# Kernel optimization log

Measured on AMD Instinct MI355X. Metric: run time of the kernel, lower is better.

Reference implementation:

```python
import jax, jax.numpy as jnp
import numpy as np

B, T, OBS, H, A, S = 4096, 64, 64, 64, 8, 201


def setup_inputs() -> dict:
    key = jax.random.key(0)
    ks = jax.random.split(key, 13)
    n = lambda k, shp, s=1.0: jax.random.normal(k, shp, dtype=jnp.float32) * s
    return {
        "x": n(ks[0], (B, T, OBS)),
        "stack": jnp.zeros((B, S, H), jnp.float32),
        "stack_ptrs": jax.random.randint(ks[1], (B, 1), 0, 100, dtype=jnp.int32),
        # core_network: init.normal_(std=1.0) per source
        "W1": n(ks[2], (H, OBS + H)), "b1": n(ks[3], (H,)),
        "W2": n(ks[4], (H, H)), "b2": n(ks[5], (H,)),
        # stack_head: default torch Linear init ~ U(-1/sqrt(H), 1/sqrt(H))
        "Ws": (jax.random.uniform(ks[6], (3, H), dtype=jnp.float32) * 2 - 1) / np.sqrt(H),
        "bs": (jax.random.uniform(ks[7], (3,), dtype=jnp.float32) * 2 - 1) / np.sqrt(H),
        # policy/value heads: init.normal_(std=0.01)
        "Wp": n(ks[8], (A, H), 0.01), "bp": n(ks[9], (A,), 0.01),
        "Wv": n(ks[10], (1, H), 0.01), "bv": n(ks[11], (1,), 0.01),
    }


def reference(x, stack, stack_ptrs, W1, b1, W2, b2, Ws, bs, Wp, bp, Wv, bv):
    # x: [B,T,OBS]  stack: [B,S,H]  stack_ptrs: [B,1] int
    batch = x.shape[0]
    bidx = jnp.arange(batch)
    ptrs0 = stack_ptrs.astype(jnp.int32)[:, 0]  # [B]

    def step(carry, x_t):
        stk, ptrs = carry
        top = stk[bidx, ptrs]                                   # [B,H] gather at ptr
        h = jnp.tanh(jnp.concatenate([x_t, top], axis=1) @ W1.T + b1)
        p = jnp.tanh(h @ W2.T + b2)                             # [B,H]
        probs = jax.nn.softmax(p @ Ws.T + bs, axis=1)           # [B,3]
        ops = jnp.argmax(probs, axis=1).astype(jnp.int32)       # 0=pop,1=noop,2=push
        push = (ops == 2)[:, None]
        # conditional scatter: write p at row ptr only where op==2
        stk = stk.at[bidx, ptrs].set(jnp.where(push, p, top))
        ptrs = jnp.maximum(ptrs + ops - 1, 0)
        logits = p @ Wp.T + bp                                  # [B,A]
        value = (p @ Wv.T + bv)[:, 0]                           # [B]
        return (stk, ptrs), (logits, value)

    (stack_out, ptrs_out), (logits_t, values_t) = jax.lax.scan(
        step, (stack, ptrs0), jnp.swapaxes(x, 0, 1))
    logitss = jnp.swapaxes(logits_t, 0, 1)      # [B,T,A]
    values = values_t.reshape(-1)               # time-major [T*B], matching torch layout
    return logitss, values, stack_out, ptrs_out[:, None]
```

## Files before the change

### kernel.cpp

```cpp
#include <hip/hip_runtime.h>
#include <cstddef>

#define NB 4096
#define NT 64
#define NOBS 64
#define NH 64
#define NA 8
#define NS 201


__device__ __forceinline__ float bl(float v, int k) {
    return __int_as_float(__builtin_amdgcn_readlane(__float_as_int(v), k));
}

__launch_bounds__(64, 2)
__global__ void stacknet_kernel(const float* __restrict__ x,
                                const float* __restrict__ stack_in,
                                const int* __restrict__ ptrs_in,
                                const float* __restrict__ W1,
                                const float* __restrict__ b1,
                                const float* __restrict__ W2,
                                const float* __restrict__ b2,
                                const float* __restrict__ Ws,
                                const float* __restrict__ bs,
                                const float* __restrict__ Wp,
                                const float* __restrict__ bp,
                                const float* __restrict__ Wv,
                                const float* __restrict__ bv,
                                float* __restrict__ logits_out,
                                float* __restrict__ values_out,
                                float* __restrict__ stack,
                                float* __restrict__ ptrs_out) {
    const int lane = threadIdx.x;
    const int jb0  = blockIdx.x * 2;
    const int jb1  = jb0 + 1;
    const int aa   = lane & 15;

    __shared__ float xcl0[28 * NH];
    __shared__ float xcl1[28 * NH];
    __shared__ __align__(16) float shw[16 * 68];
    __shared__ __align__(16) float vb0[64];
    __shared__ __align__(16) float vb1[64];

    const float* xb0 = x + (size_t)jb0 * NT * NOBS;
    const float* xb1 = x + (size_t)jb1 * NT * NOBS;
    float* stk0 = stack + (size_t)jb0 * NS * NH;
    float* stk1 = stack + (size_t)jb1 * NS * NH;

    for (int i = lane; i < 16 * 64; i += 64) {
        int a = i >> 6, k = i & 63;
        float w = (a < 3) ? Ws[a * 64 + k]
                : (a < 11) ? Wp[(a - 3) * 64 + k]
                : (a == 11) ? Wv[k] : 0.f;
        shw[a * 68 + k] = w;
    }

    {
        const float4* s40 = (const float4*)(stack_in + (size_t)jb0 * NS * NH);
        const float4* s41 = (const float4*)(stack_in + (size_t)jb1 * NS * NH);
        float4* d40 = (float4*)stk0;
        float4* d41 = (float4*)stk1;
#pragma unroll 4
        for (int i = lane; i < 164 * 16; i += 64) { d40[i] = s40[i]; d41[i] = s41[i]; }
        if (lane < 16) {
            d40[3200 + lane] = s40[3200 + lane];
            d41[3200 + lane] = s41[3200 + lane];
        }
    }

    {
        float w1x[64];
#pragma unroll
        for (int j = 0; j < 16; ++j) {
            float4 w = ((const float4*)W1)[lane * 32 + j];
            w1x[4*j] = w.x; w1x[4*j+1] = w.y; w1x[4*j+2] = w.z; w1x[4*j+3] = w.w;
        }
        float xv0 = xb0[lane], xv1 = xb1[lane];
#pragma unroll 1
        for (int t = 0; t < NT; ++t) {
            float xn0 = (t + 1 < NT) ? xb0[(t + 1) * 64 + lane] : 0.f;
            float xn1 = (t + 1 < NT) ? xb1[(t + 1) * 64 + lane] : 0.f;
            vb0[lane] = xv0;
            vb1[lane] = xv1;
            float a0 = 0.f, a1 = 0.f;
            const float4* v40 = (const float4*)vb0;
            const float4* v41 = (const float4*)vb1;
#pragma unroll
            for (int j = 0; j < 16; ++j) {
                float4 q0 = v40[j], q1 = v41[j];
                a0 = fmaf(w1x[4*j],   q0.x, a0); a1 = fmaf(w1x[4*j],   q1.x, a1);
                a0 = fmaf(w1x[4*j+1], q0.y, a0); a1 = fmaf(w1x[4*j+1], q1.y, a1);
                a0 = fmaf(w1x[4*j+2], q0.z, a0); a1 = fmaf(w1x[4*j+2], q1.z, a1);
                a0 = fmaf(w1x[4*j+3], q0.w, a0); a1 = fmaf(w1x[4*j+3], q1.w, a1);
            }
            if (t < 28) {
                xcl0[t * 64 + lane] = a0;
                xcl1[t * 64 + lane] = a1;
            } else {
                stk0[(136 + t) * 64 + lane] = a0;
                stk1[(136 + t) * 64 + lane] = a1;
            }
            xv0 = xn0; xv1 = xn1;
        }
    }

    float w1h[64], w2r[64];
#pragma unroll
    for (int j = 0; j < 16; ++j) {
        float4 wa = ((const float4*)W1)[lane * 32 + 16 + j];
        w1h[4*j] = wa.x; w1h[4*j+1] = wa.y; w1h[4*j+2] = wa.z; w1h[4*j+3] = wa.w;
        float4 wb = ((const float4*)W2)[lane * 16 + j];
        w2r[4*j] = wb.x; w2r[4*j+1] = wb.y; w2r[4*j+2] = wb.z; w2r[4*j+3] = wb.w;
    }
    float b1r  = b1[lane];
    float b2r  = b2[lane];
    float shba = (aa < 3) ? bs[aa] : (aa < 11) ? bp[aa - 3] : (aa == 11) ? bv[0] : 0.f;

    asm volatile("s_waitcnt vmcnt(0)" ::: "memory");

    int ptr0 = ptrs_in[jb0], ptr1 = ptrs_in[jb1];
    float top0 = stk0[ptr0 * 64 + lane];
    float top1 = stk1[ptr1 * 64 + lane];
    int   lA0 = -1, lA0b = -1, lA0c = -1, lA1 = -1, lA1b = -1, lA1c = -1;
    float lV0 = 0.f, lV0b = 0.f, lV0c = 0.f, lV1 = 0.f, lV1b = 0.f, lV1c = 0.f;

    float* lgb0 = logits_out + (size_t)jb0 * NT * NA;
    float* lgb1 = logits_out + (size_t)jb1 * NT * NA;

    int r00 = (ptr0 > 0) ? (ptr0 - 1) : 0;
    int r01 = (ptr1 > 0) ? (ptr1 - 1) : 0;
    float c00 = stk0[r00 * 64 + lane], c20 = stk0[(ptr0 + 1) * 64 + lane];
    float c01 = stk1[r01 * 64 + lane], c21 = stk1[(ptr1 + 1) * 64 + lane];
    float xcv0 = xcl0[lane], xcv1 = xcl1[lane];

    const float4* shwa4 = (const float4*)(shw + aa * 68);

#pragma unroll 1
    for (int t = 0; t < NT; ++t) {
        vb0[lane] = top0;
        vb1[lane] = top1;
        float acc0 = xcv0, acc1 = xcv1;
        {
            const float4* v40 = (const float4*)vb0;
            const float4* v41 = (const float4*)vb1;
#pragma unroll
            for (int j = 0; j < 16; ++j) {
                float4 q0 = v40[j], q1 = v41[j];
                acc0 = fmaf(w1h[4*j],   q0.x, acc0); acc1 = fmaf(w1h[4*j],   q1.x, acc1);
                acc0 = fmaf(w1h[4*j+1], q0.y, acc0); acc1 = fmaf(w1h[4*j+1], q1.y, acc1);
                acc0 = fmaf(w1h[4*j+2], q0.z, acc0); acc1 = fmaf(w1h[4*j+2], q1.z, acc1);
                acc0 = fmaf(w1h[4*j+3], q0.w, acc0); acc1 = fmaf(w1h[4*j+3], q1.w, acc1);
            }
        }
        float h0 = tanhf(acc0 + b1r), h1 = tanhf(acc1 + b1r);

        vb0[lane] = h0;
        vb1[lane] = h1;
        float ac20 = 0.f, ac21 = 0.f;
        {
            const float4* v40 = (const float4*)vb0;
            const float4* v41 = (const float4*)vb1;
#pragma unroll
            for (int j = 0; j < 16; ++j) {
                float4 q0 = v40[j], q1 = v41[j];
                ac20 = fmaf(w2r[4*j],   q0.x, ac20); ac21 = fmaf(w2r[4*j],   q1.x, ac21);
                ac20 = fmaf(w2r[4*j+1], q0.y, ac20); ac21 = fmaf(w2r[4*j+1], q1.y, ac21);
                ac20 = fmaf(w2r[4*j+2], q0.z, ac20); ac21 = fmaf(w2r[4*j+2], q1.z, ac21);
                ac20 = fmaf(w2r[4*j+3], q0.w, ac20); ac21 = fmaf(w2r[4*j+3], q1.w, ac21);
            }
        }
        float p0 = tanhf(ac20 + b2r), p1 = tanhf(ac21 + b2r);

        vb0[lane] = p0;
        vb1[lane] = p1;
        float hc0 = 0.f, hc1 = 0.f;
        {
            const float4* v40 = (const float4*)vb0;
            const float4* v41 = (const float4*)vb1;
#pragma unroll
            for (int j = 0; j < 16; ++j) {
                float4 wq = shwa4[j];
                float4 q0 = v40[j], q1 = v41[j];
                hc0 = fmaf(q0.x, wq.x, hc0); hc1 = fmaf(q1.x, wq.x, hc1);
                hc0 = fmaf(q0.y, wq.y, hc0); hc1 = fmaf(q1.y, wq.y, hc1);
                hc0 = fmaf(q0.z, wq.z, hc0); hc1 = fmaf(q1.z, wq.z, hc1);
                hc0 = fmaf(q0.w, wq.w, hc0); hc1 = fmaf(q1.w, wq.w, hc1);
            }
        }
        float sv0 = hc0 + shba, sv1 = hc1 + shba;

        int op0, op1;
        {
            float s0 = bl(sv0, 0), s1 = bl(sv0, 1), s2 = bl(sv0, 2);
            float mx = fmaxf(fmaxf(s0, s1), s2);
            float e0 = expf(s0 - mx), e1 = expf(s1 - mx), e2 = expf(s2 - mx);
            float S = (e0 + e1) + e2;
            float q0 = e0 / S, q1 = e1 / S, q2 = e2 / S;
            op0 = 0; float pm = q0;
            if (q1 > pm) { pm = q1; op0 = 1; }
            if (q2 > pm) { op0 = 2; }
        }
        {
            float s0 = bl(sv1, 0), s1 = bl(sv1, 1), s2 = bl(sv1, 2);
            float mx = fmaxf(fmaxf(s0, s1), s2);
            float e0 = expf(s0 - mx), e1 = expf(s1 - mx), e2 = expf(s2 - mx);
            float S = (e0 + e1) + e2;
            float q0 = e0 / S, q1 = e1 / S, q2 = e2 / S;
            op1 = 0; float pm = q0;
            if (q1 > pm) { pm = q1; op1 = 1; }
            if (q2 > pm) { op1 = 2; }
        }

        int np0 = ptr0 + op0 - 1; np0 = (np0 < 0) ? 0 : np0;
        int np1 = ptr1 + op1 - 1; np1 = (np1 < 0) ? 0 : np1;

        int nr00 = (np0 > 0) ? (np0 - 1) : 0;
        int nr01 = (np1 > 0) ? (np1 - 1) : 0;
        float nc00 = stk0[nr00 * 64 + lane];
        float nc20 = stk0[(np0 + 1) * 64 + lane];
        float nc01 = stk1[nr01 * 64 + lane];
        float nc21 = stk1[(np1 + 1) * 64 + lane];
        int tn = t + 1;
        float nxcv0, nxcv1;
        if (tn < 28) {
            nxcv0 = xcl0[tn * 64 + lane];
            nxcv1 = xcl1[tn * 64 + lane];
        } else {
            nxcv0 = stk0[(136 + tn) * 64 + lane];
            nxcv1 = stk1[(136 + tn) * 64 + lane];
        }

        if (op0 == 2) stk0[ptr0 * 64 + lane] = p0;
        if (op1 == 2) stk1[ptr1 * 64 + lane] = p1;

        float sel0;
        if (op0 == 0)
            sel0 = (r00 == lA0) ? lV0 : (r00 == lA0b) ? lV0b
                 : (r00 == lA0c) ? lV0c : c00;
        else if (op0 == 1) sel0 = top0;
        else {
            int r2 = ptr0 + 1;
            sel0 = (r2 == lA0) ? lV0 : (r2 == lA0b) ? lV0b
                 : (r2 == lA0c) ? lV0c : c20;
        }
        if (op0 == 2) { lA0c = lA0b; lV0c = lV0b; lA0b = lA0; lV0b = lV0;
                        lA0 = ptr0; lV0 = p0; }

        float sel1;
        if (op1 == 0)
            sel1 = (r01 == lA1) ? lV1 : (r01 == lA1b) ? lV1b
                 : (r01 == lA1c) ? lV1c : c01;
        else if (op1 == 1) sel1 = top1;
        else {
            int r2 = ptr1 + 1;
            sel1 = (r2 == lA1) ? lV1 : (r2 == lA1b) ? lV1b
                 : (r2 == lA1c) ? lV1c : c21;
        }
        if (op1 == 2) { lA1c = lA1b; lV1c = lV1b; lA1b = lA1; lV1b = lV1;
                        lA1 = ptr1; lV1 = p1; }

        ptr0 = np0; top0 = sel0; r00 = nr00; c00 = nc00; c20 = nc20; xcv0 = nxcv0;
        ptr1 = np1; top1 = sel1; r01 = nr01; c01 = nc01; c21 = nc21; xcv1 = nxcv1;

        if (lane >= 3 && lane <= 10) {
            lgb0[t * NA + (lane - 3)] = sv0;
            lgb1[t * NA + (lane - 3)] = sv1;
        }
        if (lane == 11) {
            values_out[(size_t)t * NB + jb0] = sv0;
            values_out[(size_t)t * NB + jb1] = sv1;
        }
    }
    if (lane == 0) {
        ptrs_out[jb0] = (float)ptr0;
        ptrs_out[jb1] = (float)ptr1;
    }

    {
        const float4* s40 = (const float4*)(stack_in + (size_t)jb0 * NS * NH);
        const float4* s41 = (const float4*)(stack_in + (size_t)jb1 * NS * NH);
        float4* d40 = (float4*)stk0;
        float4* d41 = (float4*)stk1;
#pragma unroll
        for (int i = lane; i < 576; i += 64) {
            d40[2624 + i] = s40[2624 + i];
            d41[2624 + i] = s41[2624 + i];
        }
    }
}

extern "C" void kernel_launch(void* const* d_in, const int* in_sizes, int n_in,
                              void* d_out, int out_size, void* d_ws, size_t ws_size,
                              hipStream_t stream) {
    const float* x        = (const float*)d_in[0];
    const float* stack_in = (const float*)d_in[1];
    const int*   ptrs_in  = (const int*)d_in[2];
    const float* W1 = (const float*)d_in[3];
    const float* b1 = (const float*)d_in[4];
    const float* W2 = (const float*)d_in[5];
    const float* b2 = (const float*)d_in[6];
    const float* Ws = (const float*)d_in[7];
    const float* bs = (const float*)d_in[8];
    const float* Wp = (const float*)d_in[9];
    const float* bp = (const float*)d_in[10];
    const float* Wv = (const float*)d_in[11];
    const float* bv = (const float*)d_in[12];

    float* out      = (float*)d_out;
    float* logits   = out;
    float* values   = out + 2097152;
    float* stack    = out + 2359296;
    float* ptrs_out = out + 55050240;

    stacknet_kernel<<<NB / 2, 64, 0, stream>>>(x, stack_in, ptrs_in,
                                               W1, b1, W2, b2, Ws, bs,
                                               Wp, bp, Wv, bv,
                                               logits, values, stack, ptrs_out);
}
```

Baseline: 701.1 us.

## Skew the two batch rows' recurrences so their serial stages interleave

The main loop now runs row 0 and row 1 out of phase: each fused matvec pass pairs one row's layer stage with a different stage of the other row (W2 with W1, head with W2, W1 with head). The per-step dependency chain of one row can then overlap with independent work from the other instead of both rows waiting on the same tanh/softmax/readlane points. The x-projection prologue also reads x directly from global memory with float4 loads instead of staging it through LDS, unrolled by two. The risks are higher register pressure, a longer loop body, and direct global loads in the prologue.

```diff
diff --git a/kernel.cpp b/kernel.cpp
--- a/kernel.cpp
+++ b/kernel.cpp
@@ -75,19 +75,14 @@
             float4 w = ((const float4*)W1)[lane * 32 + j];
             w1x[4*j] = w.x; w1x[4*j+1] = w.y; w1x[4*j+2] = w.z; w1x[4*j+3] = w.w;
         }
-        float xv0 = xb0[lane], xv1 = xb1[lane];
-#pragma unroll 1
+#pragma unroll 2
         for (int t = 0; t < NT; ++t) {
-            float xn0 = (t + 1 < NT) ? xb0[(t + 1) * 64 + lane] : 0.f;
-            float xn1 = (t + 1 < NT) ? xb1[(t + 1) * 64 + lane] : 0.f;
-            vb0[lane] = xv0;
-            vb1[lane] = xv1;
+            const float4* xr0 = (const float4*)(xb0 + t * 64);
+            const float4* xr1 = (const float4*)(xb1 + t * 64);
             float a0 = 0.f, a1 = 0.f;
-            const float4* v40 = (const float4*)vb0;
-            const float4* v41 = (const float4*)vb1;
 #pragma unroll
             for (int j = 0; j < 16; ++j) {
-                float4 q0 = v40[j], q1 = v41[j];
+                float4 q0 = xr0[j], q1 = xr1[j];
                 a0 = fmaf(w1x[4*j],   q0.x, a0); a1 = fmaf(w1x[4*j],   q1.x, a1);
                 a0 = fmaf(w1x[4*j+1], q0.y, a0); a1 = fmaf(w1x[4*j+1], q1.y, a1);
                 a0 = fmaf(w1x[4*j+2], q0.z, a0); a1 = fmaf(w1x[4*j+2], q1.z, a1);
@@ -100,7 +95,6 @@
                 stk0[(136 + t) * 64 + lane] = a0;
                 stk1[(136 + t) * 64 + lane] = a1;
             }
-            xv0 = xn0; xv1 = xn1;
         }
     }
 
@@ -135,45 +129,45 @@
 
     const float4* shwa4 = (const float4*)(shw + aa * 68);
 
+    float h0;
+    {
+        vb0[lane] = top0;
+        float acc0 = xcv0;
+        const float4* v40 = (const float4*)vb0;
+#pragma unroll
+        for (int j = 0; j < 16; ++j) {
+            float4 q0 = v40[j];
+            acc0 = fmaf(w1h[4*j],   q0.x, acc0);
+            acc0 = fmaf(w1h[4*j+1], q0.y, acc0);
+            acc0 = fmaf(w1h[4*j+2], q0.z, acc0);
+            acc0 = fmaf(w1h[4*j+3], q0.w, acc0);
+        }
+        h0 = tanhf(acc0 + b1r);
+    }
+
 #pragma unroll 1
     for (int t = 0; t < NT; ++t) {
-        vb0[lane] = top0;
+        vb0[lane] = h0;
         vb1[lane] = top1;
-        float acc0 = xcv0, acc1 = xcv1;
+        float ac20 = 0.f, acc1 = xcv1;
         {
             const float4* v40 = (const float4*)vb0;
             const float4* v41 = (const float4*)vb1;
 #pragma unroll
             for (int j = 0; j < 16; ++j) {
                 float4 q0 = v40[j], q1 = v41[j];
-                acc0 = fmaf(w1h[4*j],   q0.x, acc0); acc1 = fmaf(w1h[4*j],   q1.x, acc1);
-                acc0 = fmaf(w1h[4*j+1], q0.y, acc0); acc1 = fmaf(w1h[4*j+1], q1.y, acc1);
-                acc0 = fmaf(w1h[4*j+2], q0.z, acc0); acc1 = fmaf(w1h[4*j+2], q1.z, acc1);
-                acc0 = fmaf(w1h[4*j+3], q0.w, acc0); acc1 = fmaf(w1h[4*j+3], q1.w, acc1);
-            }
-        }
-        float h0 = tanhf(acc0 + b1r), h1 = tanhf(acc1 + b1r);
-
-        vb0[lane] = h0;
+                ac20 = fmaf(w2r[4*j],   q0.x, ac20); acc1 = fmaf(w1h[4*j],   q1.x, acc1);
+                ac20 = fmaf(w2r[4*j+1], q0.y, ac20); acc1 = fmaf(w1h[4*j+1], q1.y, acc1);
+                ac20 = fmaf(w2r[4*j+2], q0.z, ac20); acc1 = fmaf(w1h[4*j+2], q1.z, acc1);
+                ac20 = fmaf(w2r[4*j+3], q0.w, ac20); acc1 = fmaf(w1h[4*j+3], q1.w, acc1);
+            }
+        }
+        float p0 = tanhf(ac20 + b2r);
+        float h1 = tanhf(acc1 + b1r);
+
+        vb0[lane] = p0;
         vb1[lane] = h1;
-        float ac20 = 0.f, ac21 = 0.f;
-        {
-            const float4* v40 = (const float4*)vb0;
-            const float4* v41 = (const float4*)vb1;
-#pragma unroll
-            for (int j = 0; j < 16; ++j) {
-                float4 q0 = v40[j], q1 = v41[j];
-                ac20 = fmaf(w2r[4*j],   q0.x, ac20); ac21 = fmaf(w2r[4*j],   q1.x, ac21);
-                ac20 = fmaf(w2r[4*j+1], q0.y, ac20); ac21 = fmaf(w2r[4*j+1], q1.y, ac21);
-                ac20 = fmaf(w2r[4*j+2], q0.z, ac20); ac21 = fmaf(w2r[4*j+2], q1.z, ac21);
-                ac20 = fmaf(w2r[4*j+3], q0.w, ac20); ac21 = fmaf(w2r[4*j+3], q1.w, ac21);
-            }
-        }
-        float p0 = tanhf(ac20 + b2r), p1 = tanhf(ac21 + b2r);
-
-        vb0[lane] = p0;
-        vb1[lane] = p1;
-        float hc0 = 0.f, hc1 = 0.f;
+        float hc0 = 0.f, ac21 = 0.f;
         {
             const float4* v40 = (const float4*)vb0;
             const float4* v41 = (const float4*)vb1;
@@ -181,15 +175,16 @@
             for (int j = 0; j < 16; ++j) {
                 float4 wq = shwa4[j];
                 float4 q0 = v40[j], q1 = v41[j];
-                hc0 = fmaf(q0.x, wq.x, hc0); hc1 = fmaf(q1.x, wq.x, hc1);
-                hc0 = fmaf(q0.y, wq.y, hc0); hc1 = fmaf(q1.y, wq.y, hc1);
-                hc0 = fmaf(q0.z, wq.z, hc0); hc1 = fmaf(q1.z, wq.z, hc1);
-                hc0 = fmaf(q0.w, wq.w, hc0); hc1 = fmaf(q1.w, wq.w, hc1);
-            }
-        }
-        float sv0 = hc0 + shba, sv1 = hc1 + shba;
-
-        int op0, op1;
+                hc0 = fmaf(q0.x, wq.x, hc0); ac21 = fmaf(w2r[4*j],   q1.x, ac21);
+                hc0 = fmaf(q0.y, wq.y, hc0); ac21 = fmaf(w2r[4*j+1], q1.y, ac21);
+                hc0 = fmaf(q0.z, wq.z, hc0); ac21 = fmaf(w2r[4*j+2], q1.z, ac21);
+                hc0 = fmaf(q0.w, wq.w, hc0); ac21 = fmaf(w2r[4*j+3], q1.w, ac21);
+            }
+        }
+        float sv0 = hc0 + shba;
+        float p1 = tanhf(ac21 + b2r);
+
+        int op0;
         {
             float s0 = bl(sv0, 0), s1 = bl(sv0, 1), s2 = bl(sv0, 2);
             float mx = fmaxf(fmaxf(s0, s1), s2);
@@ -200,38 +195,16 @@
             if (q1 > pm) { pm = q1; op0 = 1; }
             if (q2 > pm) { op0 = 2; }
         }
-        {
-            float s0 = bl(sv1, 0), s1 = bl(sv1, 1), s2 = bl(sv1, 2);
-            float mx = fmaxf(fmaxf(s0, s1), s2);
-            float e0 = expf(s0 - mx), e1 = expf(s1 - mx), e2 = expf(s2 - mx);
-            float S = (e0 + e1) + e2;
-            float q0 = e0 / S, q1 = e1 / S, q2 = e2 / S;
-            op1 = 0; float pm = q0;
-            if (q1 > pm) { pm = q1; op1 = 1; }
-            if (q2 > pm) { op1 = 2; }
-        }
-
         int np0 = ptr0 + op0 - 1; np0 = (np0 < 0) ? 0 : np0;
-        int np1 = ptr1 + op1 - 1; np1 = (np1 < 0) ? 0 : np1;
 
         int nr00 = (np0 > 0) ? (np0 - 1) : 0;
-        int nr01 = (np1 > 0) ? (np1 - 1) : 0;
         float nc00 = stk0[nr00 * 64 + lane];
         float nc20 = stk0[(np0 + 1) * 64 + lane];
-        float nc01 = stk1[nr01 * 64 + lane];
-        float nc21 = stk1[(np1 + 1) * 64 + lane];
         int tn = t + 1;
-        float nxcv0, nxcv1;
-        if (tn < 28) {
-            nxcv0 = xcl0[tn * 64 + lane];
-            nxcv1 = xcl1[tn * 64 + lane];
-        } else {
-            nxcv0 = stk0[(136 + tn) * 64 + lane];
-            nxcv1 = stk1[(136 + tn) * 64 + lane];
-        }
+        float nxcv0 = (tn < 28) ? xcl0[tn * 64 + lane]
+                                : stk0[(136 + tn) * 64 + lane];
 
         if (op0 == 2) stk0[ptr0 * 64 + lane] = p0;
-        if (op1 == 2) stk1[ptr1 * 64 + lane] = p1;
 
         float sel0;
         if (op0 == 0)
@@ -245,6 +218,50 @@
         }
         if (op0 == 2) { lA0c = lA0b; lV0c = lV0b; lA0b = lA0; lV0b = lV0;
                         lA0 = ptr0; lV0 = p0; }
+        ptr0 = np0; top0 = sel0; r00 = nr00; c00 = nc00; c20 = nc20; xcv0 = nxcv0;
+
+        if (lane >= 3 && lane <= 10) lgb0[t * NA + (lane - 3)] = sv0;
+        if (lane == 11) values_out[(size_t)t * NB + jb0] = sv0;
+
+        vb0[lane] = top0;
+        vb1[lane] = p1;
+        float acc0 = xcv0, hc1 = 0.f;
+        {
+            const float4* v40 = (const float4*)vb0;
+            const float4* v41 = (const float4*)vb1;
+#pragma unroll
+            for (int j = 0; j < 16; ++j) {
+                float4 wq = shwa4[j];
+                float4 q0 = v40[j], q1 = v41[j];
+                acc0 = fmaf(w1h[4*j],   q0.x, acc0); hc1 = fmaf(q1.x, wq.x, hc1);
+                acc0 = fmaf(w1h[4*j+1], q0.y, acc0); hc1 = fmaf(q1.y, wq.y, hc1);
+                acc0 = fmaf(w1h[4*j+2], q0.z, acc0); hc1 = fmaf(q1.z, wq.z, hc1);
+                acc0 = fmaf(w1h[4*j+3], q0.w, acc0); hc1 = fmaf(q1.w, wq.w, hc1);
+            }
+        }
+        h0 = tanhf(acc0 + b1r);
+        float sv1 = hc1 + shba;
+
+        int op1;
+        {
+            float s0 = bl(sv1, 0), s1 = bl(sv1, 1), s2 = bl(sv1, 2);
+            float mx = fmaxf(fmaxf(s0, s1), s2);
+            float e0 = expf(s0 - mx), e1 = expf(s1 - mx), e2 = expf(s2 - mx);
+            float S = (e0 + e1) + e2;
+            float q0 = e0 / S, q1 = e1 / S, q2 = e2 / S;
+            op1 = 0; float pm = q0;
+            if (q1 > pm) { pm = q1; op1 = 1; }
+            if (q2 > pm) { op1 = 2; }
+        }
+        int np1 = ptr1 + op1 - 1; np1 = (np1 < 0) ? 0 : np1;
+
+        int nr01 = (np1 > 0) ? (np1 - 1) : 0;
+        float nc01 = stk1[nr01 * 64 + lane];
+        float nc21 = stk1[(np1 + 1) * 64 + lane];
+        float nxcv1 = (tn < 28) ? xcl1[tn * 64 + lane]
+                                : stk1[(136 + tn) * 64 + lane];
+
+        if (op1 == 2) stk1[ptr1 * 64 + lane] = p1;
 
         float sel1;
         if (op1 == 0)
@@ -258,18 +275,10 @@
         }
         if (op1 == 2) { lA1c = lA1b; lV1c = lV1b; lA1b = lA1; lV1b = lV1;
                         lA1 = ptr1; lV1 = p1; }
-
-        ptr0 = np0; top0 = sel0; r00 = nr00; c00 = nc00; c20 = nc20; xcv0 = nxcv0;
         ptr1 = np1; top1 = sel1; r01 = nr01; c01 = nc01; c21 = nc21; xcv1 = nxcv1;
 
-        if (lane >= 3 && lane <= 10) {
-            lgb0[t * NA + (lane - 3)] = sv0;
-            lgb1[t * NA + (lane - 3)] = sv1;
-        }
-        if (lane == 11) {
-            values_out[(size_t)t * NB + jb0] = sv0;
-            values_out[(size_t)t * NB + jb1] = sv1;
-        }
+        if (lane >= 3 && lane <= 10) lgb1[t * NA + (lane - 3)] = sv1;
+        if (lane == 11) values_out[(size_t)t * NB + jb1] = sv1;
     }
     if (lane == 0) {
         ptrs_out[jb0] = (float)ptr0;
```

Measured after the change: 1.002 ms. +43.0%, slower.
